# Kernel optimization log

Measured on AMD Instinct MI355X. Metric: run time of the kernel, lower is better.

The kernel has to match this reference:

```python
import jax, jax.numpy as jnp
import numpy as np

# physics constants (match PDELoss defaults)
RHO, CP, VZ, KT = 0.3, 1200.0, 0.5, 0.06
# Arrhenius-style soot source constants (representative RadiationPINN.soot_source_terms)
A_NUC, E_NUC = 1.0e4, 2.0e4
A_GROW, E_GROW = 5.0e3, 1.2e4
A_OX, E_OX = 1.0e5, 1.6e4

N, IN_DIM, H, OUT, N_FUELS, EMB = 262144, 12, 128, 7, 4, 8


def mlp(X, emb_rows, W1, b1, W2, b2, W3, b3, Wo, bo):
    # X: (N,4) coords; emb_rows: (N,8) fuel embedding -> T (N,1), fv (N,1), Y (N,5)
    h = jnp.concatenate([X, emb_rows], axis=-1)
    h = jnp.tanh(h @ W1 + b1)
    h = jnp.tanh(h @ W2 + b2)
    h = jnp.tanh(h @ W3 + b3)
    o = h @ Wo + bo
    T = 300.0 + 2000.0 * jax.nn.sigmoid(o[:, 0:1])
    fv = jax.nn.softplus(o[:, 1:2]) * 1e-6
    Y = jax.nn.softmax(o[:, 2:7], axis=-1)
    return T, fv, Y


def soot_sources(T, Y_prec, Y_O2, fv):
    nuc = A_NUC * Y_prec * jnp.exp(-E_NUC / T)
    grow = A_GROW * Y_prec * fv * jnp.exp(-E_GROW / T)
    ox = A_OX * Y_O2 * fv * jnp.sqrt(T) * jnp.exp(-E_OX / T)
    return nuc, grow, ox


def pde_loss(inputs, fuel_ids, W1, b1, W2, b2, W3, b3, Wo, bo, emb):
    emb_rows = emb[fuel_ids]  # (N, EMB), constant w.r.t. inputs
    params = (W1, b1, W2, b2, W3, b3, Wo, bo)

    def T_of(X):
        return mlp(X, emb_rows, *params)[0]

    def fv_of(X):
        return mlp(X, emb_rows, *params)[1]

    n = inputs.shape[0]
    Ez = jnp.zeros_like(inputs).at[:, 1].set(1.0)  # direction d/dz
    Er = jnp.zeros_like(inputs).at[:, 2].set(1.0)  # direction d/dr

    # forward-mode (Taylor) derivatives: nested jvp gives 1st and 2nd order in one pass
    dT_dz_fn = lambda X: jax.jvp(T_of, (X,), (Ez,))[1]
    dT_dz, d2T_dz2 = jax.jvp(dT_dz_fn, (inputs,), (Ez,))
    dT_dr_fn = lambda X: jax.jvp(T_of, (X,), (Er,))[1]
    dT_dr, d2T_dr2 = jax.jvp(dT_dr_fn, (inputs,), (Er,))
    _, dfv_dz = jax.jvp(fv_of, (inputs,), (Ez,))

    T, fv, Y = mlp(inputs, emb_rows, *params)
    Y_prec, Y_O2 = Y[:, 3:4], Y[:, 4:5]

    r = inputs[:, 2:3]
    r_safe = jnp.maximum(r, 1e-6)
    laplacian_r = d2T_dr2 + dT_dr / r_safe
    energy_res = RHO * CP * VZ * dT_dz - KT * laplacian_r - KT * d2T_dz2

    nuc, grow, ox = soot_sources(T, Y_prec, Y_O2, fv)
    soot_res = VZ * dfv_dz - nuc - grow + ox

    loss_energy = jnp.mean(energy_res ** 2)
    loss_soot = jnp.mean(soot_res ** 2)
    return jnp.stack([loss_energy, loss_soot, loss_energy + loss_soot])


def setup_inputs() -> dict:
    key = jax.random.key(0)
    ks = jax.random.split(key, 12)
    inputs = jax.random.uniform(ks[0], (N, 4), dtype=jnp.float32)
    fuel_ids = jax.random.randint(ks[1], (N,), 0, N_FUELS)
    s1, sh, so = 1.0 / np.sqrt(IN_DIM), 1.0 / np.sqrt(H), 1.0 / np.sqrt(H)
    return {
        "inputs": inputs,
        "fuel_ids": fuel_ids,
        "W1": jax.random.normal(ks[2], (IN_DIM, H), jnp.float32) * s1,
        "b1": jnp.zeros((H,), jnp.float32),
        "W2": jax.random.normal(ks[3], (H, H), jnp.float32) * sh,
        "b2": jnp.zeros((H,), jnp.float32),
        "W3": jax.random.normal(ks[4], (H, H), jnp.float32) * sh,
        "b3": jnp.zeros((H,), jnp.float32),
        "Wo": jax.random.normal(ks[5], (H, OUT), jnp.float32) * so,
        "bo": jnp.zeros((OUT,), jnp.float32),
        "emb": jax.random.normal(ks[6], (N_FUELS, EMB), jnp.float32) * 0.1,
    }


def reference(inputs, fuel_ids, W1, b1, W2, b2, W3, b3, Wo, bo, emb):
    return pde_loss(inputs, fuel_ids, W1, b1, W2, b2, W3, b3, Wo, bo, emb)
```

## Files before the change

kernel.cpp:

```cpp
#include <hip/hip_runtime.h>
#include <math.h>

#define NPTS 262144
#define PTS  16
#define NBLK (NPTS / PTS)
#define AP   136

typedef _Float16 f16;
typedef f16    f16x4 __attribute__((ext_vector_type(4)));
typedef f16    f16x8 __attribute__((ext_vector_type(8)));
typedef __fp16 h16x2 __attribute__((ext_vector_type(2)));
typedef __fp16 h16x4 __attribute__((ext_vector_type(4)));
typedef float  f32x4 __attribute__((ext_vector_type(4)));


__device__ __forceinline__ h16x2 pk(float a, float b) {
    return __builtin_amdgcn_cvt_pkrtz(a, b);
}
__device__ __forceinline__ f16x4 mrg(h16x2 lo, h16x2 hi) {
    h16x4 v = __builtin_shufflevector(lo, hi, 0, 1, 2, 3);
    return __builtin_bit_cast(f16x4, v);
}

__device__ __forceinline__ float fast_tanh(float z) {
    float e = __expf(2.f * z);
    return 1.f - __fdividef(2.f, e + 1.f);
}

__global__ void prep_weights(const float* __restrict__ W1, const float* __restrict__ W2,
                             const float* __restrict__ W3, const float* __restrict__ Wo,
                             const float* __restrict__ bo,
                             f16* __restrict__ wt1, f16* __restrict__ wt2,
                             f16* __restrict__ wt3, f16* __restrict__ wot,
                             float* __restrict__ bot)
{
    int tid    = blockIdx.x * blockDim.x + threadIdx.x;
    int stride = gridDim.x * blockDim.x;
    for (int i = tid; i < 128 * 32; i += stride) {
        int k = i >> 7, n = i & 127;
        wt1[n * 32 + k] = (f16)((k < 12) ? W1[k * 128 + n] : 0.f);
    }
    for (int i = tid; i < 128 * 128; i += stride) {
        int k = i >> 7, n = i & 127;
        wt2[n * 128 + k] = (f16)W2[i];
        wt3[n * 128 + k] = (f16)W3[i];
    }
    for (int i = tid; i < 16 * 128; i += stride) {
        int k = i >> 4, n = i & 15;
        wot[n * 128 + k] = (f16)((n < 7) ? Wo[k * 7 + n] : 0.f);
    }
    if (tid < 16) bot[tid] = (tid < 7) ? bo[tid] : 0.f;
}

__device__ __forceinline__ void transform_store(
    f16 (*sAct)[PTS][AP], const f32x4 acc[5], const f32x4 bv,
    int pt, int n0q)
{
    float t[4], s[4];
#pragma unroll
    for (int r = 0; r < 4; ++r) {
        float z = acc[0][r] + bv[r];
        t[r] = fast_tanh(z);
        s[r] = 1.f - t[r] * t[r];
    }
    h16x2 T[2]  = { pk(t[0], t[1]), pk(t[2], t[3]) };
    h16x2 S[2]  = { pk(s[0], s[1]), pk(s[2], s[3]) };
    h16x2 A1[2] = { pk(acc[1][0], acc[1][1]), pk(acc[1][2], acc[1][3]) };
    h16x2 A2[2] = { pk(acc[2][0], acc[2][1]), pk(acc[2][2], acc[2][3]) };
    h16x2 A3[2] = { pk(acc[3][0], acc[3][1]), pk(acc[3][2], acc[3][3]) };
    h16x2 A4[2] = { pk(acc[4][0], acc[4][1]), pk(acc[4][2], acc[4][3]) };
    h16x2 TZ[2], TZZ[2], TR[2], TRR[2];
#pragma unroll
    for (int p = 0; p < 2; ++p) {
        h16x2 n2t = -(T[p] + T[p]);
        TZ[p]  = S[p] * A1[p];
        TR[p]  = S[p] * A3[p];
        TZZ[p] = n2t * (TZ[p] * A1[p]) + S[p] * A2[p];
        TRR[p] = n2t * (TR[p] * A3[p]) + S[p] * A4[p];
    }
    *(f16x4*)&sAct[0][pt][n0q] = mrg(T[0], T[1]);
    *(f16x4*)&sAct[1][pt][n0q] = mrg(TZ[0], TZ[1]);
    *(f16x4*)&sAct[2][pt][n0q] = mrg(TZZ[0], TZZ[1]);
    *(f16x4*)&sAct[3][pt][n0q] = mrg(TR[0], TR[1]);
    *(f16x4*)&sAct[4][pt][n0q] = mrg(TRR[0], TRR[1]);
}

__device__ __forceinline__ void layer128(
    f16 (*sAct)[PTS][AP], const f16* __restrict__ Wt, const float* __restrict__ b,
    int half, int q, int m)
{
    f16x8 Bv[5][4];
#pragma unroll
    for (int c = 0; c < 5; ++c)
#pragma unroll
        for (int kt = 0; kt < 4; ++kt)
            Bv[c][kt] = *(const f16x8*)&sAct[c][m][kt * 32 + q * 8];
    __syncthreads();

    const f32x4 z4 = {0.f, 0.f, 0.f, 0.f};
#pragma unroll
    for (int ct0 = 0; ct0 < 4; ++ct0) {
        const int n0 = (half * 4 + ct0) * 16;
        const f16* wp = &Wt[(n0 + m) * 128 + q * 8];
        f16x8 A0 = *(const f16x8*)(wp);
        f16x8 A1 = *(const f16x8*)(wp + 32);
        f16x8 A2 = *(const f16x8*)(wp + 64);
        f16x8 A3 = *(const f16x8*)(wp + 96);
        f32x4 bb = *(const f32x4*)&b[n0 + q * 4];
        f32x4 acc[5];
#pragma unroll
        for (int c = 0; c < 5; ++c) acc[c] = __builtin_amdgcn_mfma_f32_16x16x32_f16(A0, Bv[c][0], z4, 0, 0, 0);
#pragma unroll
        for (int c = 0; c < 5; ++c) acc[c] = __builtin_amdgcn_mfma_f32_16x16x32_f16(A1, Bv[c][1], acc[c], 0, 0, 0);
#pragma unroll
        for (int c = 0; c < 5; ++c) acc[c] = __builtin_amdgcn_mfma_f32_16x16x32_f16(A2, Bv[c][2], acc[c], 0, 0, 0);
#pragma unroll
        for (int c = 0; c < 5; ++c) acc[c] = __builtin_amdgcn_mfma_f32_16x16x32_f16(A3, Bv[c][3], acc[c], 0, 0, 0);

        transform_store(sAct, acc, bb, m, n0 + q * 4);
    }
    __syncthreads();
}

__global__ __launch_bounds__(128, 2) void pde_main(
    const float* __restrict__ X,
    const int*   __restrict__ fid,
    const float* __restrict__ emb,
    const float* __restrict__ b1, const float* __restrict__ b2,
    const float* __restrict__ b3,
    const f16* __restrict__ Wt1, const f16* __restrict__ Wt2,
    const f16* __restrict__ Wt3, const f16* __restrict__ Wot,
    const float* __restrict__ bot,
    float* __restrict__ partials)
{
    __shared__ f32x4 smem4[5 * PTS * AP * 2 / 16];
    __shared__ float sRes[PTS][2];
    f16   (*sAct)[PTS][AP] = (f16(*)[PTS][AP])smem4;
    float (*sO)[PTS][17]   = (float(*)[PTS][17])smem4;

    const int tid  = threadIdx.x;
    const int half = tid >> 6;
    const int lane = tid & 63;
    const int q    = lane >> 4;
    const int m    = lane & 15;
    const int p0   = blockIdx.x * PTS;

    {
        const f32x4 z4 = {0.f, 0.f, 0.f, 0.f};
        for (int i = tid; i < 5 * PTS * 4; i += 128) {
            int row = i >> 2;
            int seg = i & 3;
            int c = row >> 4, p = row & 15;
            *(f32x4*)&sAct[c][p][seg * 8] = z4;
        }
    }
    __syncthreads();
    if (tid < PTS) {
        const int p = tid;
        f32x4 xr = *(const f32x4*)&X[(p0 + p) * 4];
        const float* er = &emb[fid[p0 + p] * 8];
        f32x4 e0 = *(const f32x4*)er;
        f32x4 e1 = *(const f32x4*)(er + 4);
        *(f16x4*)&sAct[0][p][0] = mrg(pk(xr.x, xr.y), pk(xr.z, xr.w));
        *(f16x4*)&sAct[0][p][4] = mrg(pk(e0.x, e0.y), pk(e0.z, e0.w));
        *(f16x4*)&sAct[0][p][8] = mrg(pk(e1.x, e1.y), pk(e1.z, e1.w));
        sAct[1][p][1] = (f16)1.f;
        sAct[3][p][2] = (f16)1.f;
    }
    __syncthreads();

    {
        f16x8 Bv[5];
#pragma unroll
        for (int c = 0; c < 5; ++c)
            Bv[c] = *(const f16x8*)&sAct[c][m][q * 8];
        __syncthreads();
        const f32x4 z4 = {0.f, 0.f, 0.f, 0.f};
#pragma unroll
        for (int ct0 = 0; ct0 < 4; ++ct0) {
            const int n0 = (half * 4 + ct0) * 16;
            f16x8 A0 = *(const f16x8*)&Wt1[(n0 + m) * 32 + q * 8];
            f32x4 bb = *(const f32x4*)&b1[n0 + q * 4];
            f32x4 acc[5];
#pragma unroll
            for (int c = 0; c < 5; ++c)
                acc[c] = __builtin_amdgcn_mfma_f32_16x16x32_f16(A0, Bv[c], z4, 0, 0, 0);
            transform_store(sAct, acc, bb, m, n0 + q * 4);
        }
        __syncthreads();
    }

    layer128(sAct, Wt2, b2, half, q, m);
    layer128(sAct, Wt3, b3, half, q, m);

    f16x8 Bh[5][4];
    f32x4 boq = {0.f, 0.f, 0.f, 0.f};
    if (half == 0) {
#pragma unroll
        for (int c = 0; c < 5; ++c)
#pragma unroll
            for (int kt = 0; kt < 4; ++kt)
                Bh[c][kt] = *(const f16x8*)&sAct[c][m][kt * 32 + q * 8];
        boq = *(const f32x4*)&bot[q * 4];
    }
    __syncthreads();
    if (half == 0) {
        const f16* wp = &Wot[m * 128 + q * 8];
        f16x8 A0 = *(const f16x8*)(wp);
        f16x8 A1 = *(const f16x8*)(wp + 32);
        f16x8 A2 = *(const f16x8*)(wp + 64);
        f16x8 A3 = *(const f16x8*)(wp + 96);
        const f32x4 z4 = {0.f, 0.f, 0.f, 0.f};
        f32x4 acc[5];
#pragma unroll
        for (int c = 0; c < 5; ++c) acc[c] = __builtin_amdgcn_mfma_f32_16x16x32_f16(A0, Bh[c][0], z4, 0, 0, 0);
#pragma unroll
        for (int c = 0; c < 5; ++c) acc[c] = __builtin_amdgcn_mfma_f32_16x16x32_f16(A1, Bh[c][1], acc[c], 0, 0, 0);
#pragma unroll
        for (int c = 0; c < 5; ++c) acc[c] = __builtin_amdgcn_mfma_f32_16x16x32_f16(A2, Bh[c][2], acc[c], 0, 0, 0);
#pragma unroll
        for (int c = 0; c < 5; ++c) acc[c] = __builtin_amdgcn_mfma_f32_16x16x32_f16(A3, Bh[c][3], acc[c], 0, 0, 0);
#pragma unroll
        for (int c = 0; c < 5; ++c)
#pragma unroll
            for (int r = 0; r < 4; ++r)
                sO[c][m][q * 4 + r] = acc[c][r] + ((c == 0) ? boq[r] : 0.f);
    }
    __syncthreads();

    if (tid < PTS) {
        const int pt = tid;
        float o0   = sO[0][pt][0], o1  = sO[0][pt][1];
        float o0z  = sO[1][pt][0], o1z = sO[1][pt][1];
        float o0zz = sO[2][pt][0];
        float o0r  = sO[3][pt][0];
        float o0rr = sO[4][pt][0];

        float sg  = __fdividef(1.f, 1.f + __expf(-o0));
        float T   = 300.f + 2000.f * sg;
        float sp  = sg * (1.f - sg);
        float spp = sp * (1.f - 2.f * sg);
        float Tz  = 2000.f * sp * o0z;
        float Tzz = 2000.f * (spp * o0z * o0z + sp * o0zz);
        float Tr  = 2000.f * sp * o0r;
        float Trr = 2000.f * (spp * o0r * o0r + sp * o0rr);

        float fv  = ((o1 > 20.f) ? o1 : __logf(1.f + __expf(o1))) * 1e-6f;
        float s1  = __fdividef(1.f, 1.f + __expf(-o1));
        float fvz = s1 * o1z * 1e-6f;

        float y0 = sO[0][pt][2], y1 = sO[0][pt][3], y2 = sO[0][pt][4];
        float y3 = sO[0][pt][5], y4 = sO[0][pt][6];
        float mx = fmaxf(fmaxf(fmaxf(y0, y1), fmaxf(y2, y3)), y4);
        float e0 = __expf(y0 - mx), e1 = __expf(y1 - mx), e2 = __expf(y2 - mx);
        float e3 = __expf(y3 - mx), e4 = __expf(y4 - mx);
        float inv = __fdividef(1.f, e0 + e1 + e2 + e3 + e4);
        float Yp = e3 * inv;
        float Yo = e4 * inv;

        float r   = X[(p0 + pt) * 4 + 2];
        float rs  = fmaxf(r, 1e-6f);
        float rT  = __fdividef(1.f, T);
        float lap = Trr + __fdividef(Tr, rs);
        float eres = 180.f * Tz - 0.06f * lap - 0.06f * Tzz;

        float nuc  = 1e4f * Yp * __expf(-20000.f * rT);
        float grow = 5e3f * Yp * fv * __expf(-12000.f * rT);
        float ox   = 1e5f * Yo * fv * sqrtf(T) * __expf(-16000.f * rT);
        float sres = 0.5f * fvz - nuc - grow + ox;

        sRes[pt][0] = eres * eres;
        sRes[pt][1] = sres * sres;
    }
    __syncthreads();
    if (tid == 0) {
        float se = 0.f, ss = 0.f;
#pragma unroll
        for (int p = 0; p < PTS; ++p) { se += sRes[p][0]; ss += sRes[p][1]; }
        partials[2 * blockIdx.x]     = se;
        partials[2 * blockIdx.x + 1] = ss;
    }
}

__global__ __launch_bounds__(1024) void pde_finalize(
    const float* __restrict__ partials, float* __restrict__ out)
{
    __shared__ double rE[1024];
    __shared__ double rS[1024];
    const int tid = threadIdx.x;
    const float2* p2 = (const float2*)partials;
    double se = 0.0, ss = 0.0;
    for (int i = tid; i < NBLK; i += 1024) {
        float2 v = p2[i];
        se += (double)v.x;
        ss += (double)v.y;
    }
    rE[tid] = se; rS[tid] = ss;
    __syncthreads();
    for (int s = 512; s > 0; s >>= 1) {
        if (tid < s) { rE[tid] += rE[tid + s]; rS[tid] += rS[tid + s]; }
        __syncthreads();
    }
    if (tid == 0) {
        const double invN = 1.0 / (double)NPTS;
        float le = (float)(rE[0] * invN);
        float ls = (float)(rS[0] * invN);
        out[0] = le;
        out[1] = ls;
        out[2] = le + ls;
    }
}

extern "C" void kernel_launch(void* const* d_in, const int* in_sizes, int n_in,
                              void* d_out, int out_size, void* d_ws, size_t ws_size,
                              hipStream_t stream)
{
    const float* X   = (const float*)d_in[0];
    const int*   fid = (const int*)  d_in[1];
    const float* W1  = (const float*)d_in[2];
    const float* b1  = (const float*)d_in[3];
    const float* W2  = (const float*)d_in[4];
    const float* b2  = (const float*)d_in[5];
    const float* W3  = (const float*)d_in[6];
    const float* b3  = (const float*)d_in[7];
    const float* Wo  = (const float*)d_in[8];
    const float* bo  = (const float*)d_in[9];
    const float* emb = (const float*)d_in[10];

    f16*   wt1      = (f16*)d_ws;
    f16*   wt2      = wt1 + 128 * 32;
    f16*   wt3      = wt2 + 128 * 128;
    f16*   wot      = wt3 + 128 * 128;
    float* bot      = (float*)(wot + 16 * 128);
    float* partials = bot + 16;
    float* out      = (float*)d_out;

    prep_weights<<<128, 256, 0, stream>>>(W1, W2, W3, Wo, bo, wt1, wt2, wt3, wot, bot);
    pde_main<<<NBLK, 128, 0, stream>>>(X, fid, emb, b1, b2, b3,
                                       wt1, wt2, wt3, wot, bot, partials);
    pde_finalize<<<1, 1024, 0, stream>>>(partials, out);
}
```

Before: 252.3 us.

## Exploit constant tangents in layer 1, fold biases into MFMA, split output head

```diff
diff --git a/kernel.cpp b/kernel.cpp
--- a/kernel.cpp
+++ b/kernel.cpp
@@ -24,7 +24,8 @@
 
 __device__ __forceinline__ float fast_tanh(float z) {
     float e = __expf(2.f * z);
-    return 1.f - __fdividef(2.f, e + 1.f);
+    float r = __builtin_amdgcn_rcpf(e + 1.f);
+    return __builtin_fmaf(-2.f, r, 1.f);
 }
 
 __global__ void prep_weights(const float* __restrict__ W1, const float* __restrict__ W2,
@@ -53,14 +54,12 @@
 }
 
 __device__ __forceinline__ void transform_store(
-    f16 (*sAct)[PTS][AP], const f32x4 acc[5], const f32x4 bv,
-    int pt, int n0q)
+    f16 (*sAct)[PTS][AP], const f32x4 acc[5], int pt, int n0q)
 {
     float t[4], s[4];
 #pragma unroll
     for (int r = 0; r < 4; ++r) {
-        float z = acc[0][r] + bv[r];
-        t[r] = fast_tanh(z);
+        t[r] = fast_tanh(acc[0][r]);
         s[r] = 1.f - t[r] * t[r];
     }
     h16x2 T[2]  = { pk(t[0], t[1]), pk(t[2], t[3]) };
@@ -77,6 +76,36 @@
         TR[p]  = S[p] * A3[p];
         TZZ[p] = n2t * (TZ[p] * A1[p]) + S[p] * A2[p];
         TRR[p] = n2t * (TR[p] * A3[p]) + S[p] * A4[p];
+    }
+    *(f16x4*)&sAct[0][pt][n0q] = mrg(T[0], T[1]);
+    *(f16x4*)&sAct[1][pt][n0q] = mrg(TZ[0], TZ[1]);
+    *(f16x4*)&sAct[2][pt][n0q] = mrg(TZZ[0], TZZ[1]);
+    *(f16x4*)&sAct[3][pt][n0q] = mrg(TR[0], TR[1]);
+    *(f16x4*)&sAct[4][pt][n0q] = mrg(TRR[0], TRR[1]);
+}
+
+__device__ __forceinline__ void transform_store_l1(
+    f16 (*sAct)[PTS][AP], const f32x4 acc0, const f32x4 wz, const f32x4 wr,
+    int pt, int n0q)
+{
+    float t[4], s[4];
+#pragma unroll
+    for (int r = 0; r < 4; ++r) {
+        t[r] = fast_tanh(acc0[r]);
+        s[r] = 1.f - t[r] * t[r];
+    }
+    h16x2 T[2]  = { pk(t[0], t[1]), pk(t[2], t[3]) };
+    h16x2 S[2]  = { pk(s[0], s[1]), pk(s[2], s[3]) };
+    h16x2 A1[2] = { pk(wz[0], wz[1]), pk(wz[2], wz[3]) };
+    h16x2 A3[2] = { pk(wr[0], wr[1]), pk(wr[2], wr[3]) };
+    h16x2 TZ[2], TZZ[2], TR[2], TRR[2];
+#pragma unroll
+    for (int p = 0; p < 2; ++p) {
+        h16x2 n2t = -(T[p] + T[p]);
+        TZ[p]  = S[p] * A1[p];
+        TR[p]  = S[p] * A3[p];
+        TZZ[p] = n2t * (TZ[p] * A1[p]);
+        TRR[p] = n2t * (TR[p] * A3[p]);
     }
     *(f16x4*)&sAct[0][pt][n0q] = mrg(T[0], T[1]);
     *(f16x4*)&sAct[1][pt][n0q] = mrg(TZ[0], TZ[1]);
@@ -108,8 +137,9 @@
         f16x8 A3 = *(const f16x8*)(wp + 96);
         f32x4 bb = *(const f32x4*)&b[n0 + q * 4];
         f32x4 acc[5];
-#pragma unroll
-        for (int c = 0; c < 5; ++c) acc[c] = __builtin_amdgcn_mfma_f32_16x16x32_f16(A0, Bv[c][0], z4, 0, 0, 0);
+        acc[0] = __builtin_amdgcn_mfma_f32_16x16x32_f16(A0, Bv[0][0], bb, 0, 0, 0);
+#pragma unroll
+        for (int c = 1; c < 5; ++c) acc[c] = __builtin_amdgcn_mfma_f32_16x16x32_f16(A0, Bv[c][0], z4, 0, 0, 0);
 #pragma unroll
         for (int c = 0; c < 5; ++c) acc[c] = __builtin_amdgcn_mfma_f32_16x16x32_f16(A1, Bv[c][1], acc[c], 0, 0, 0);
 #pragma unroll
@@ -117,7 +147,7 @@
 #pragma unroll
         for (int c = 0; c < 5; ++c) acc[c] = __builtin_amdgcn_mfma_f32_16x16x32_f16(A3, Bv[c][3], acc[c], 0, 0, 0);
 
-        transform_store(sAct, acc, bb, m, n0 + q * 4);
+        transform_store(sAct, acc, m, n0 + q * 4);
     }
     __syncthreads();
 }
@@ -126,6 +156,7 @@
     const float* __restrict__ X,
     const int*   __restrict__ fid,
     const float* __restrict__ emb,
+    const float* __restrict__ W1,
     const float* __restrict__ b1, const float* __restrict__ b2,
     const float* __restrict__ b3,
     const f16* __restrict__ Wt1, const f16* __restrict__ Wt2,
@@ -134,7 +165,6 @@
     float* __restrict__ partials)
 {
     __shared__ f32x4 smem4[5 * PTS * AP * 2 / 16];
-    __shared__ float sRes[PTS][2];
     f16   (*sAct)[PTS][AP] = (f16(*)[PTS][AP])smem4;
     float (*sO)[PTS][17]   = (float(*)[PTS][17])smem4;
 
@@ -145,47 +175,36 @@
     const int m    = lane & 15;
     const int p0   = blockIdx.x * PTS;
 
-    {
-        const f32x4 z4 = {0.f, 0.f, 0.f, 0.f};
-        for (int i = tid; i < 5 * PTS * 4; i += 128) {
-            int row = i >> 2;
-            int seg = i & 3;
-            int c = row >> 4, p = row & 15;
-            *(f32x4*)&sAct[c][p][seg * 8] = z4;
-        }
-    }
-    __syncthreads();
     if (tid < PTS) {
         const int p = tid;
         f32x4 xr = *(const f32x4*)&X[(p0 + p) * 4];
         const float* er = &emb[fid[p0 + p] * 8];
         f32x4 e0 = *(const f32x4*)er;
         f32x4 e1 = *(const f32x4*)(er + 4);
-        *(f16x4*)&sAct[0][p][0] = mrg(pk(xr.x, xr.y), pk(xr.z, xr.w));
-        *(f16x4*)&sAct[0][p][4] = mrg(pk(e0.x, e0.y), pk(e0.z, e0.w));
-        *(f16x4*)&sAct[0][p][8] = mrg(pk(e1.x, e1.y), pk(e1.z, e1.w));
-        sAct[1][p][1] = (f16)1.f;
-        sAct[3][p][2] = (f16)1.f;
+        const f16x4 zz = {(f16)0.f, (f16)0.f, (f16)0.f, (f16)0.f};
+        *(f16x4*)&sAct[0][p][0]  = mrg(pk(xr.x, xr.y), pk(xr.z, xr.w));
+        *(f16x4*)&sAct[0][p][4]  = mrg(pk(e0.x, e0.y), pk(e0.z, e0.w));
+        *(f16x4*)&sAct[0][p][8]  = mrg(pk(e1.x, e1.y), pk(e1.z, e1.w));
+        *(f16x4*)&sAct[0][p][12] = zz;
+        *(f16x4*)&sAct[0][p][16] = zz;
+        *(f16x4*)&sAct[0][p][20] = zz;
+        *(f16x4*)&sAct[0][p][24] = zz;
+        *(f16x4*)&sAct[0][p][28] = zz;
     }
     __syncthreads();
 
     {
-        f16x8 Bv[5];
-#pragma unroll
-        for (int c = 0; c < 5; ++c)
-            Bv[c] = *(const f16x8*)&sAct[c][m][q * 8];
+        f16x8 Bv0 = *(const f16x8*)&sAct[0][m][q * 8];
         __syncthreads();
-        const f32x4 z4 = {0.f, 0.f, 0.f, 0.f};
 #pragma unroll
         for (int ct0 = 0; ct0 < 4; ++ct0) {
             const int n0 = (half * 4 + ct0) * 16;
             f16x8 A0 = *(const f16x8*)&Wt1[(n0 + m) * 32 + q * 8];
             f32x4 bb = *(const f32x4*)&b1[n0 + q * 4];
-            f32x4 acc[5];
-#pragma unroll
-            for (int c = 0; c < 5; ++c)
-                acc[c] = __builtin_amdgcn_mfma_f32_16x16x32_f16(A0, Bv[c], z4, 0, 0, 0);
-            transform_store(sAct, acc, bb, m, n0 + q * 4);
+            f32x4 acc0 = __builtin_amdgcn_mfma_f32_16x16x32_f16(A0, Bv0, bb, 0, 0, 0);
+            f32x4 wz = *(const f32x4*)&W1[128 + n0 + q * 4];
+            f32x4 wr = *(const f32x4*)&W1[256 + n0 + q * 4];
+            transform_store_l1(sAct, acc0, wz, wr, m, n0 + q * 4);
         }
         __syncthreads();
     }
@@ -193,92 +212,87 @@
     layer128(sAct, Wt2, b2, half, q, m);
     layer128(sAct, Wt3, b3, half, q, m);
 
-    f16x8 Bh[5][4];
-    f32x4 boq = {0.f, 0.f, 0.f, 0.f};
-    if (half == 0) {
-#pragma unroll
-        for (int c = 0; c < 5; ++c)
-#pragma unroll
-            for (int kt = 0; kt < 4; ++kt)
-                Bh[c][kt] = *(const f16x8*)&sAct[c][m][kt * 32 + q * 8];
-        boq = *(const f32x4*)&bot[q * 4];
-    }
-    __syncthreads();
-    if (half == 0) {
+    const int nch = 3 - half;
+    const int cb  = half * 3;
+    f16x8 Bh[3][4];
+#pragma unroll
+    for (int c = 0; c < 3; ++c) if (c < nch)
+#pragma unroll
+        for (int kt = 0; kt < 4; ++kt)
+            Bh[c][kt] = *(const f16x8*)&sAct[cb + c][m][kt * 32 + q * 8];
+    f32x4 c0i = {0.f, 0.f, 0.f, 0.f};
+    if (half == 0) c0i = *(const f32x4*)&bot[q * 4];
+    __syncthreads();
+    {
         const f16* wp = &Wot[m * 128 + q * 8];
         f16x8 A0 = *(const f16x8*)(wp);
         f16x8 A1 = *(const f16x8*)(wp + 32);
         f16x8 A2 = *(const f16x8*)(wp + 64);
         f16x8 A3 = *(const f16x8*)(wp + 96);
         const f32x4 z4 = {0.f, 0.f, 0.f, 0.f};
-        f32x4 acc[5];
-#pragma unroll
-        for (int c = 0; c < 5; ++c) acc[c] = __builtin_amdgcn_mfma_f32_16x16x32_f16(A0, Bh[c][0], z4, 0, 0, 0);
-#pragma unroll
-        for (int c = 0; c < 5; ++c) acc[c] = __builtin_amdgcn_mfma_f32_16x16x32_f16(A1, Bh[c][1], acc[c], 0, 0, 0);
-#pragma unroll
-        for (int c = 0; c < 5; ++c) acc[c] = __builtin_amdgcn_mfma_f32_16x16x32_f16(A2, Bh[c][2], acc[c], 0, 0, 0);
-#pragma unroll
-        for (int c = 0; c < 5; ++c) acc[c] = __builtin_amdgcn_mfma_f32_16x16x32_f16(A3, Bh[c][3], acc[c], 0, 0, 0);
-#pragma unroll
-        for (int c = 0; c < 5; ++c)
+        f32x4 acc[3];
+#pragma unroll
+        for (int c = 0; c < 3; ++c) if (c < nch) acc[c] = __builtin_amdgcn_mfma_f32_16x16x32_f16(A0, Bh[c][0], (c == 0) ? c0i : z4, 0, 0, 0);
+#pragma unroll
+        for (int c = 0; c < 3; ++c) if (c < nch) acc[c] = __builtin_amdgcn_mfma_f32_16x16x32_f16(A1, Bh[c][1], acc[c], 0, 0, 0);
+#pragma unroll
+        for (int c = 0; c < 3; ++c) if (c < nch) acc[c] = __builtin_amdgcn_mfma_f32_16x16x32_f16(A2, Bh[c][2], acc[c], 0, 0, 0);
+#pragma unroll
+        for (int c = 0; c < 3; ++c) if (c < nch) acc[c] = __builtin_amdgcn_mfma_f32_16x16x32_f16(A3, Bh[c][3], acc[c], 0, 0, 0);
+#pragma unroll
+        for (int c = 0; c < 3; ++c) if (c < nch)
 #pragma unroll
             for (int r = 0; r < 4; ++r)
-                sO[c][m][q * 4 + r] = acc[c][r] + ((c == 0) ? boq[r] : 0.f);
-    }
-    __syncthreads();
-
-    if (tid < PTS) {
-        const int pt = tid;
-        float o0   = sO[0][pt][0], o1  = sO[0][pt][1];
-        float o0z  = sO[1][pt][0], o1z = sO[1][pt][1];
-        float o0zz = sO[2][pt][0];
-        float o0r  = sO[3][pt][0];
-        float o0rr = sO[4][pt][0];
-
-        float sg  = __fdividef(1.f, 1.f + __expf(-o0));
-        float T   = 300.f + 2000.f * sg;
-        float sp  = sg * (1.f - sg);
-        float spp = sp * (1.f - 2.f * sg);
-        float Tz  = 2000.f * sp * o0z;
-        float Tzz = 2000.f * (spp * o0z * o0z + sp * o0zz);
-        float Tr  = 2000.f * sp * o0r;
-        float Trr = 2000.f * (spp * o0r * o0r + sp * o0rr);
-
-        float fv  = ((o1 > 20.f) ? o1 : __logf(1.f + __expf(o1))) * 1e-6f;
-        float s1  = __fdividef(1.f, 1.f + __expf(-o1));
-        float fvz = s1 * o1z * 1e-6f;
-
-        float y0 = sO[0][pt][2], y1 = sO[0][pt][3], y2 = sO[0][pt][4];
-        float y3 = sO[0][pt][5], y4 = sO[0][pt][6];
-        float mx = fmaxf(fmaxf(fmaxf(y0, y1), fmaxf(y2, y3)), y4);
-        float e0 = __expf(y0 - mx), e1 = __expf(y1 - mx), e2 = __expf(y2 - mx);
-        float e3 = __expf(y3 - mx), e4 = __expf(y4 - mx);
-        float inv = __fdividef(1.f, e0 + e1 + e2 + e3 + e4);
-        float Yp = e3 * inv;
-        float Yo = e4 * inv;
-
-        float r   = X[(p0 + pt) * 4 + 2];
-        float rs  = fmaxf(r, 1e-6f);
-        float rT  = __fdividef(1.f, T);
-        float lap = Trr + __fdividef(Tr, rs);
-        float eres = 180.f * Tz - 0.06f * lap - 0.06f * Tzz;
-
-        float nuc  = 1e4f * Yp * __expf(-20000.f * rT);
-        float grow = 5e3f * Yp * fv * __expf(-12000.f * rT);
-        float ox   = 1e5f * Yo * fv * sqrtf(T) * __expf(-16000.f * rT);
-        float sres = 0.5f * fvz - nuc - grow + ox;
-
-        sRes[pt][0] = eres * eres;
-        sRes[pt][1] = sres * sres;
-    }
-    __syncthreads();
-    if (tid == 0) {
-        float se = 0.f, ss = 0.f;
-#pragma unroll
-        for (int p = 0; p < PTS; ++p) { se += sRes[p][0]; ss += sRes[p][1]; }
-        partials[2 * blockIdx.x]     = se;
-        partials[2 * blockIdx.x + 1] = ss;
+                sO[cb + c][m][q * 4 + r] = acc[c][r];
+    }
+    __syncthreads();
+
+    if (lane < PTS) {
+        const int pt = lane;
+        float o0 = sO[0][pt][0];
+        float sg = __fdividef(1.f, 1.f + __expf(-o0));
+        float v;
+        if (half == 0) {
+            float o0z  = sO[1][pt][0];
+            float o0zz = sO[2][pt][0];
+            float o0r  = sO[3][pt][0];
+            float o0rr = sO[4][pt][0];
+            float sp  = sg * (1.f - sg);
+            float spp = sp * (1.f - 2.f * sg);
+            float Tz  = 2000.f * sp * o0z;
+            float Tzz = 2000.f * (spp * o0z * o0z + sp * o0zz);
+            float Tr  = 2000.f * sp * o0r;
+            float Trr = 2000.f * (spp * o0r * o0r + sp * o0rr);
+            float r   = X[(p0 + pt) * 4 + 2];
+            float rs  = fmaxf(r, 1e-6f);
+            float lap = Trr + __fdividef(Tr, rs);
+            float eres = 180.f * Tz - 0.06f * lap - 0.06f * Tzz;
+            v = eres * eres;
+        } else {
+            float o1  = sO[0][pt][1];
+            float o1z = sO[1][pt][1];
+            float T   = 300.f + 2000.f * sg;
+            float fv  = ((o1 > 20.f) ? o1 : __logf(1.f + __expf(o1))) * 1e-6f;
+            float s1  = __fdividef(1.f, 1.f + __expf(-o1));
+            float fvz = s1 * o1z * 1e-6f;
+            float y0 = sO[0][pt][2], y1 = sO[0][pt][3], y2 = sO[0][pt][4];
+            float y3 = sO[0][pt][5], y4 = sO[0][pt][6];
+            float mx = fmaxf(fmaxf(fmaxf(y0, y1), fmaxf(y2, y3)), y4);
+            float e0 = __expf(y0 - mx), e1 = __expf(y1 - mx), e2 = __expf(y2 - mx);
+            float e3 = __expf(y3 - mx), e4 = __expf(y4 - mx);
+            float inv = __fdividef(1.f, e0 + e1 + e2 + e3 + e4);
+            float Yp = e3 * inv;
+            float Yo = e4 * inv;
+            float rT  = __fdividef(1.f, T);
+            float nuc  = 1e4f * Yp * __expf(-20000.f * rT);
+            float grow = 5e3f * Yp * fv * __expf(-12000.f * rT);
+            float ox   = 1e5f * Yo * fv * sqrtf(T) * __expf(-16000.f * rT);
+            float sres = 0.5f * fvz - nuc - grow + ox;
+            v = sres * sres;
+        }
+#pragma unroll
+        for (int o = 8; o > 0; o >>= 1) v += __shfl_xor(v, o, 64);
+        if (pt == 0) partials[2 * blockIdx.x + half] = v;
     }
 }
 
@@ -336,7 +350,7 @@
     float* out      = (float*)d_out;
 
     prep_weights<<<128, 256, 0, stream>>>(W1, W2, W3, Wo, bo, wt1, wt2, wt3, wot, bot);
-    pde_main<<<NBLK, 128, 0, stream>>>(X, fid, emb, b1, b2, b3,
+    pde_main<<<NBLK, 128, 0, stream>>>(X, fid, emb, W1, b1, b2, b3,
                                        wt1, wt2, wt3, wot, bot, partials);
     pde_finalize<<<1, 1024, 0, stream>>>(partials, out);
 }
```

Result: slower. 261.7 us (+3.7%).
